# Optimization experiments

Measured on AMD Instinct MI355X. Metric: run time of the kernel, lower is better.

The kernel has to match this reference:

```python
import jax, jax.numpy as jnp
import numpy as np

GRID_SIZE = 5
SPLINE_ORDER = 3
COUPLING = 0.05
LN_EPS = 1e-5
BATCH = 1024
IN_DIM = 2048
HIDDEN = [4096, 4096, 2048]


def _knots():
    k = SPLINE_ORDER
    return np.concatenate([np.full(k, -1.0), np.linspace(-1.0, 1.0, GRID_SIZE + 1), np.full(k, 1.0)])


def bspline_basis(t):
    # Replicates the module's partial in-place Cox-de Boor recursion exactly:
    # after the loops, cols[0..4] are degree-3, col 5 degree-2, col 6 degree-1, col 7 degree-0.
    knots = _knots()
    k = SPLINE_ORDER
    n = len(knots) - k - 1  # 8
    cols = [jnp.where((t >= knots[i]) & (t < knots[i + 1]), 1.0, 0.0).astype(t.dtype)
            for i in range(min(n, len(knots) - 1))]
    for degree in range(1, min(k + 1, n)):
        for i in range(n - degree):
            denom1 = knots[i + degree] - knots[i]
            denom2 = knots[i + degree + 1] - knots[i + 1]
            term1 = ((t - knots[i]) / denom1) * cols[i] if denom1 > 1e-10 else 0.0
            term2 = (((knots[i + degree + 1] - t) / denom2) * cols[i + 1]
                     if (denom2 > 1e-10 and i + 1 < n) else 0.0)
            cols[i] = term1 + term2
    return jnp.stack(cols, axis=-1)  # [..., n]


def kan_activation(x, control_points, reg_weights):
    # x: [B, D]; control_points: [D, grid+order+1]; reg_weights: [D]
    t = jnp.tanh(x)
    basis = bspline_basis(t)  # [B, D, n]
    m = min(basis.shape[-1], control_points.shape[1])  # min(8, 9) = 8
    spline = jnp.einsum('bdn,dn->bd', basis[..., :m], control_points[:, :m])
    return jnp.clip(spline * reg_weights[None, :], -10.0, 10.0)


def _generators():
    sx = np.array([[0., 1.], [1., 0.]], np.float32)
    sy = np.array([[0., -1.], [1., 0.]], np.float32)
    sz = np.array([[1., 0.], [0., -1.]], np.float32)
    return np.stack([sx, sy, sz, np.eye(2, dtype=np.float32)])  # [4,2,2]

GENS = jnp.asarray(_generators())
GEN_DIAG = jnp.asarray(np.stack([np.diagonal(g) for g in _generators()]))  # [4,2]


def noncommutative_transform(x):
    # pairs of the flattened tensor, generator index cycles mod 4
    shape = x.shape
    flat = x.reshape(-1)
    P = flat.shape[0] // 2
    vec = flat[:2 * P].reshape(P, 2)
    ng = GENS.shape[0]
    if P % ng == 0:
        v = vec.reshape(P // ng, ng, 2)                      # [Q, 4, 2]
        gv = jnp.einsum('gij,qgj->qgi', GENS, v)
        vg = v * GEN_DIAG[None, :, :]
        comm = jnp.clip(gv - vg, -1.0, 1.0)
        out = (v + COUPLING * comm).reshape(-1)
    else:
        G = GENS[jnp.arange(P) % ng]
        gv = jnp.einsum('pij,pj->pi', G, vec)
        vg = vec * jnp.diagonal(G, axis1=-2, axis2=-1)
        comm = jnp.clip(gv - vg, -1.0, 1.0)
        out = (vec + COUPLING * comm).reshape(-1)
    if flat.shape[0] % 2 == 1:
        out = jnp.concatenate([out, flat[-1:]])
    return out.reshape(shape)


def setup_inputs() -> dict:
    key = jax.random.key(0)
    ks = jax.random.split(key, 16)
    inp = {'x': jax.random.normal(ks[0], (BATCH, IN_DIM), jnp.float32)}
    prev = IN_DIM
    ncp = GRID_SIZE + SPLINE_ORDER + 1  # 9
    for li, h in enumerate(HIDDEN, start=1):
        kw, kb, kc = jax.random.split(ks[li], 3)
        inp[f'W{li}'] = jax.random.normal(kw, (h, prev), jnp.float32) / np.sqrt(prev)
        inp[f'b{li}'] = jnp.zeros((h,), jnp.float32)
        inp[f'cp{li}'] = jax.random.normal(kc, (h, ncp), jnp.float32) * 0.1
        inp[f'rw{li}'] = jnp.full((h,), 0.5, jnp.float32)
        prev = h
    inp['W_out'] = jax.random.normal(ks[10], (IN_DIM, prev), jnp.float32) / np.sqrt(prev)
    inp['b_out'] = jnp.zeros((IN_DIM,), jnp.float32)
    return inp


def reference(x, W1, b1, cp1, rw1, W2, b2, cp2, rw2, W3, b3, cp3, rw3, W_out, b_out):
    # F.layer_norm over feature dim, no affine
    mu = jnp.mean(x, axis=-1, keepdims=True)
    var = jnp.var(x, axis=-1, keepdims=True)
    cur = (x - mu) / jnp.sqrt(var + LN_EPS)
    for W, b, cp, rw in ((W1, b1, cp1, rw1), (W2, b2, cp2, rw2), (W3, b3, cp3, rw3)):
        lin = cur @ W.T + b
        kan = kan_activation(lin, cp, rw)
        cur = noncommutative_transform(kan)  # dropout = identity in eval
    return cur @ W_out.T + b_out
```

## Files before the change

kernel.cpp:

```cpp
#include <hip/hip_runtime.h>

typedef __attribute__((ext_vector_type(8))) short bf16x8;
typedef __attribute__((ext_vector_type(4))) float f32x4;

__device__ __forceinline__ float b2f(unsigned short u) {
    union { unsigned int i; float f; } x; x.i = ((unsigned int)u) << 16; return x.f;
}
__device__ __forceinline__ unsigned short f2b(float f) {
    union { float f; unsigned int i; } x; x.f = f;
    unsigned int r = x.i + 0x7fffu + ((x.i >> 16) & 1u);
    return (unsigned short)(r >> 16);
}

__device__ __forceinline__ void gl16(unsigned short* l, const unsigned short* g) {
    __builtin_amdgcn_global_load_lds((__attribute__((address_space(1))) void*)g,
                                     (__attribute__((address_space(3))) void*)l, 16, 0, 0);
}

__device__ __forceinline__ float kan_spline(float t, const float* cpf, float rwf) {
    float c3 = (t >= -1.0f && t < -0.6f) ? 1.0f : 0.0f;
    float c4 = (t >= -0.6f && t < -0.2f) ? 1.0f : 0.0f;
    float c5 = (t >= -0.2f && t <  0.2f) ? 1.0f : 0.0f;
    float c6 = (t >=  0.2f && t <  0.6f) ? 1.0f : 0.0f;
    float c7 = (t >=  0.6f && t <  1.0f) ? 1.0f : 0.0f;
    float d2 = (-0.6f - t) * 2.5f * c3;
    float d3 = (t + 1.0f) * 2.5f * c3 + (-0.2f - t) * 2.5f * c4;
    float d4 = (t + 0.6f) * 2.5f * c4 + ( 0.2f - t) * 2.5f * c5;
    float d5 = (t + 0.2f) * 2.5f * c5 + ( 0.6f - t) * 2.5f * c6;
    float d6 = (t - 0.2f) * 2.5f * c6 + ( 1.0f - t) * 2.5f * c7;
    float e1 = (-0.6f - t) * 2.5f  * d2;
    float e2 = (t + 1.0f) * 2.5f  * d2 + (-0.2f - t) * 1.25f * d3;
    float e3 = (t + 1.0f) * 1.25f * d3 + ( 0.2f - t) * 1.25f * d4;
    float e4 = (t + 0.6f) * 1.25f * d4 + ( 0.6f - t) * 1.25f * d5;
    float e5 = (t + 0.2f) * 1.25f * d5 + ( 1.0f - t) * 1.25f * d6;
    const float r12 = 1.0f / 1.2f;
    float f0 = (-0.6f - t) * 2.5f  * e1;
    float f1 = (t + 1.0f) * 2.5f  * e1 + (-0.2f - t) * 1.25f * e2;
    float f2 = (t + 1.0f) * 1.25f * e2 + ( 0.2f - t) * r12   * e3;
    float f3 = (t + 1.0f) * r12   * e3 + ( 0.6f - t) * r12   * e4;
    float f4 = (t + 0.6f) * r12   * e4 + ( 1.0f - t) * r12   * e5;
    float sp = f0*cpf[0] + f1*cpf[1] + f2*cpf[2] + f3*cpf[3] + f4*cpf[4]
             + e5*cpf[5] + d6*cpf[6] + c7*cpf[7];
    float v = sp * rwf;
    return fminf(fmaxf(v, -10.0f), 10.0f);
}

__global__ void ln_stats_kernel(const float* __restrict__ x,
                                float* __restrict__ mu, float* __restrict__ rstd) {
    const int row = blockIdx.x;
    const float* p = x + (size_t)row * 2048 + threadIdx.x * 8;
    double s = 0.0, q = 0.0;
#pragma unroll
    for (int i = 0; i < 8; ++i) { float v = p[i]; s += v; q += (double)v * v; }
    for (int o = 32; o > 0; o >>= 1) { s += __shfl_down(s, o, 64); q += __shfl_down(q, o, 64); }
    __shared__ double shs[4], shq[4];
    const int lane = threadIdx.x & 63, w = threadIdx.x >> 6;
    if (lane == 0) { shs[w] = s; shq[w] = q; }
    __syncthreads();
    if (threadIdx.x == 0) {
        double S = shs[0] + shs[1] + shs[2] + shs[3];
        double Q = shq[0] + shq[1] + shq[2] + shq[3];
        double m = S / 2048.0;
        double var = Q / 2048.0 - m * m;
        mu[row] = (float)m;
        rstd[row] = (float)(1.0 / sqrt(var + 1e-5));
    }
}

__global__ void rowsum_kernel(const float* __restrict__ W,
                              float* __restrict__ S, int K) {
    const int lane = threadIdx.x & 63, w = threadIdx.x >> 6;
    const int row = blockIdx.x * 4 + w;
    const float* p = W + (size_t)row * K;
    double s = 0.0;
    for (int c = lane * 8; c < K; c += 512) {
#pragma unroll
        for (int i = 0; i < 8; ++i) s += p[c + i];
    }
    for (int o = 32; o > 0; o >>= 1) s += __shfl_down(s, o, 64);
    if (lane == 0) S[row] = (float)s;
}

__global__ void split2_kernel(const float* __restrict__ src,
                              unsigned short* __restrict__ dst, int C) {
    const int r = blockIdx.x;
    const int c = threadIdx.x * 8;
    const float* p = src + (size_t)r * C + c;
    float4 u0 = ((const float4*)p)[0];
    float4 u1 = ((const float4*)p)[1];
    float v[8] = {u0.x, u0.y, u0.z, u0.w, u1.x, u1.y, u1.z, u1.w};
    unsigned short hi[8], lo[8];
#pragma unroll
    for (int i = 0; i < 8; ++i) {
        hi[i] = f2b(v[i]);
        lo[i] = f2b(v[i] - b2f(hi[i]));
    }
    unsigned short* d = dst + (size_t)r * 2 * C + c;
    *(uint4*)d = *(const uint4*)hi;
    *(uint4*)(d + C) = *(const uint4*)lo;
}

__global__ void pre_all(const float* __restrict__ x, const float* __restrict__ W1,
                        float* __restrict__ mu, float* __restrict__ rstd,
                        float* __restrict__ S1,
                        unsigned short* __restrict__ Asplit,
                        unsigned short* __restrict__ W1b) {
    const int tid = threadIdx.x;
    const int lane = tid & 63, w = tid >> 6;
    const int c = tid * 8;
    __shared__ double shs[4], shq[4];
    if (blockIdx.x < 1024) {
        const int r = blockIdx.x;
        const float* p = x + (size_t)r * 2048 + c;
        float4 u0 = ((const float4*)p)[0];
        float4 u1 = ((const float4*)p)[1];
        float v[8] = {u0.x, u0.y, u0.z, u0.w, u1.x, u1.y, u1.z, u1.w};
        double s = 0.0, q = 0.0;
#pragma unroll
        for (int i = 0; i < 8; ++i) { s += v[i]; q += (double)v[i] * v[i]; }
        for (int o = 32; o > 0; o >>= 1) { s += __shfl_down(s, o, 64); q += __shfl_down(q, o, 64); }
        if (lane == 0) { shs[w] = s; shq[w] = q; }
        __syncthreads();
        if (tid == 0) {
            double S = shs[0] + shs[1] + shs[2] + shs[3];
            double Q = shq[0] + shq[1] + shq[2] + shq[3];
            double m = S / 2048.0;
            double var = Q / 2048.0 - m * m;
            mu[r] = (float)m;
            rstd[r] = (float)(1.0 / sqrt(var + 1e-5));
        }
        unsigned short hi[8], lo[8];
#pragma unroll
        for (int i = 0; i < 8; ++i) {
            hi[i] = f2b(v[i]);
            lo[i] = f2b(v[i] - b2f(hi[i]));
        }
        unsigned short* d = Asplit + (size_t)r * 4096 + c;
        *(uint4*)d = *(const uint4*)hi;
        *(uint4*)(d + 2048) = *(const uint4*)lo;
    } else {
        const int r = blockIdx.x - 1024;
        const float* p = W1 + (size_t)r * 2048 + c;
        float4 u0 = ((const float4*)p)[0];
        float4 u1 = ((const float4*)p)[1];
        float v[8] = {u0.x, u0.y, u0.z, u0.w, u1.x, u1.y, u1.z, u1.w};
        double s = 0.0;
#pragma unroll
        for (int i = 0; i < 8; ++i) s += v[i];
        for (int o = 32; o > 0; o >>= 1) s += __shfl_down(s, o, 64);
        if (lane == 0) shs[w] = s;
        __syncthreads();
        if (tid == 0) S1[r] = (float)(shs[0] + shs[1] + shs[2] + shs[3]);
        unsigned short hi[8], lo[8];
#pragma unroll
        for (int i = 0; i < 8; ++i) {
            hi[i] = f2b(v[i]);
            lo[i] = f2b(v[i] - b2f(hi[i]));
        }
        unsigned short* d = W1b + (size_t)r * 4096 + c;
        *(uint4*)d = *(const uint4*)hi;
        *(uint4*)(d + 2048) = *(const uint4*)lo;
    }
}

__global__ void cvt_kernel(const float* __restrict__ src,
                           unsigned short* __restrict__ dst) {
    const size_t i = ((size_t)blockIdx.x * 256 + threadIdx.x) * 8;
    float4 u0 = ((const float4*)(src + i))[0];
    float4 u1 = ((const float4*)(src + i))[1];
    float v[8] = {u0.x, u0.y, u0.z, u0.w, u1.x, u1.y, u1.z, u1.w};
    unsigned short t[8];
#pragma unroll
    for (int q = 0; q < 8; ++q) t[q] = f2b(v[q]);
    *(uint4*)(dst + i) = *(const uint4*)t;
}

__global__ void cvt2_kernel(const float* __restrict__ s1, unsigned short* __restrict__ d1,
                            int nb1, const float* __restrict__ s2,
                            unsigned short* __restrict__ d2) {
    const int b = blockIdx.x;
    const float* src = (b < nb1) ? s1 : s2;
    unsigned short* dst = (b < nb1) ? d1 : d2;
    const int bb = (b < nb1) ? b : b - nb1;
    const size_t i = ((size_t)bb * 256 + threadIdx.x) * 8;
    float4 u0 = ((const float4*)(src + i))[0];
    float4 u1 = ((const float4*)(src + i))[1];
    float v[8] = {u0.x, u0.y, u0.z, u0.w, u1.x, u1.y, u1.z, u1.w};
    unsigned short t[8];
#pragma unroll
    for (int q = 0; q < 8; ++q) t[q] = f2b(v[q]);
    *(uint4*)(dst + i) = *(const uint4*)t;
}

__global__ __launch_bounds__(512, 4)
void gemm_kan1(const unsigned short* __restrict__ Ab,
               const unsigned short* __restrict__ Bb,
               const float* __restrict__ bias, const float* __restrict__ cp,
               const float* __restrict__ rw, const float* __restrict__ mu,
               const float* __restrict__ rstd, const float* __restrict__ S1,
               unsigned short* __restrict__ outp,
               int Nld, int Klog, int lda, int ldb)
{
    constexpr int BM = 64, BN = 128;
    constexpr int ABASE = 0, BBASE = 4096;
    constexpr int BUF = 12288;
    __shared__ unsigned short lds[3 * BUF];

    const int tid  = threadIdx.x;
    const int lane = tid & 63;
    const int wid  = tid >> 6;

    const int gx = gridDim.x;
    int flat = blockIdx.y * gx + blockIdx.x;
    const int nwg = gx * gridDim.y;
    if ((nwg & 7) == 0) flat = (flat & 7) * (nwg >> 3) + (flat >> 3);
    const int bm = (flat % gx) * BM;
    const int bn = (flat / gx) * BN;

    const int wmo = (wid >> 2) * 32;
    const int wno = (wid & 3) * 32;
    const int fr = lane & 15;
    const int kq = lane >> 4;
    const int sxr = fr & 7;

    const int uA0 = tid;
    const int uB0 = tid, uB1 = tid + 512;
#define VLOG(u) ((((u) & 7)) ^ (((u) >> 3) & 7))
#define SRCC(u) (((VLOG(u) & 3) << 3) + ((VLOG(u) >> 2) * 2048))
    const size_t aoff0 = (size_t)(bm + (uA0 >> 3)) * lda + SRCC(uA0);
    const size_t boff0 = (size_t)(bn + (uB0 >> 3)) * ldb + SRCC(uB0);
    const size_t boff1 = (size_t)(bn + (uB1 >> 3)) * ldb + SRCC(uB1);
#undef SRCC
#undef VLOG

    f32x4 acc[2][2] = {};

#define STAGE(BSEL, K) do {                                           \
    unsigned short* l_ = &lds[(BSEL) * BUF];                          \
    gl16(l_ + ABASE + uA0 * 8, Ab + aoff0 + (K));                     \
    gl16(l_ + BBASE + uB0 * 8, Bb + boff0 + (K));                     \
    gl16(l_ + BBASE + uB1 * 8, Bb + boff1 + (K));                     \
} while (0)

    const int nt = Klog / 32;
    STAGE(0, 0);
    STAGE(1, 32);

    for (int t = 0; t < nt; ++t) {
        if (t + 1 < nt) asm volatile("s_waitcnt vmcnt(3)" ::: "memory");
        else            asm volatile("s_waitcnt vmcnt(0)" ::: "memory");
        __builtin_amdgcn_s_barrier();
        __builtin_amdgcn_sched_barrier(0);
        if (t + 2 < nt) STAGE((t + 2) % 3, (t + 2) * 32);
        const unsigned short* cl = &lds[(t % 3) * BUF];
        const int slH = ((kq ^ sxr)) << 3;
        const int slL = (((4 + kq) ^ sxr)) << 3;
        bf16x8 aH[2], aL[2], bH[2], bL[2];
#pragma unroll
        for (int i = 0; i < 2; ++i) {
            const int ro = ABASE + (wmo + i * 16 + fr) * 64;
            aH[i] = *(const bf16x8*)&cl[ro + slH];
            aL[i] = *(const bf16x8*)&cl[ro + slL];
        }
#pragma unroll
        for (int j = 0; j < 2; ++j) {
            const int ro = BBASE + (wno + j * 16 + fr) * 64;
            bH[j] = *(const bf16x8*)&cl[ro + slH];
            bL[j] = *(const bf16x8*)&cl[ro + slL];
        }
#pragma unroll
        for (int i = 0; i < 2; ++i)
#pragma unroll
            for (int j = 0; j < 2; ++j)
                acc[i][j] = __builtin_amdgcn_mfma_f32_16x16x32_bf16(aH[i], bH[j], acc[i][j], 0, 0, 0);
#pragma unroll
        for (int i = 0; i < 2; ++i)
#pragma unroll
            for (int j = 0; j < 2; ++j)
                acc[i][j] = __builtin_amdgcn_mfma_f32_16x16x32_bf16(aL[i], bH[j], acc[i][j], 0, 0, 0);
#pragma unroll
        for (int i = 0; i < 2; ++i)
#pragma unroll
            for (int j = 0; j < 2; ++j)
                acc[i][j] = __builtin_amdgcn_mfma_f32_16x16x32_bf16(aH[i], bL[j], acc[i][j], 0, 0, 0);
    }
#undef STAGE

    const int rowg = (lane >> 4) * 4;
#pragma unroll
    for (int j = 0; j < 2; ++j) {
        const int n = bn + wno + j * 16 + fr;
        const float bs = bias[n];
        float cpf[8];
#pragma unroll
        for (int q = 0; q < 8; ++q) cpf[q] = cp[(size_t)n * 9 + q];
        const float rwf = rw[n];
        const float s1 = S1[n];
        const int s = n & 7;
#pragma unroll
        for (int i = 0; i < 2; ++i) {
            const int m0 = bm + wmo + i * 16 + rowg;
#pragma unroll
            for (int r = 0; r < 4; ++r) {
                const int m = m0 + r;
                float v = acc[i][j][r];
                v = (v - mu[m] * s1) * rstd[m] + bs;
                v = kan_spline(tanhf(v), cpf, rwf);
                float p = __shfl_xor(v, 1, 64);
                p = fminf(fmaxf(p, -1.0f), 1.0f);
                if (s < 4) v += ((s == 2) ? -0.05f : 0.05f) * p;
                outp[(size_t)m * Nld + n] = f2b(v);
            }
        }
    }
}

template <int EPI>
__global__ __launch_bounds__(256, 2)
void gemm_kan2(const unsigned short* __restrict__ Ab,
               const unsigned short* __restrict__ Bb,
               const float* __restrict__ bias, const float* __restrict__ cp,
               const float* __restrict__ rw, const float* __restrict__ mu,
               const float* __restrict__ rstd, const float* __restrict__ S1,
               void* __restrict__ outp,
               int Nld, int n0, int Ktot, int lda, int ldb)
{
    constexpr int BM = 64, BN = 128, BK = 64;
    constexpr int ASZ = BM * BK;
    constexpr int BUF = ASZ + BN * BK;
    __shared__ unsigned short lds[3 * BUF];

    const int tid  = threadIdx.x;
    const int lane = tid & 63;
    const int wid  = tid >> 6;

    const int gx = gridDim.x;
    int flat = blockIdx.y * gx + blockIdx.x;
    const int nwg = gx * gridDim.y;
    if ((nwg & 7) == 0) flat = (flat & 7) * (nwg >> 3) + (flat >> 3);
    const int bm = (flat % gx) * BM;
    const int bn = (flat / gx) * BN;

    const int wmo = (wid >> 1) * 32;
    const int wno = (wid & 1) * 64;
    const int fr = lane & 15;
    const int kq = lane >> 4;
    const int sxr = fr & 7;

    const int uA0 = (wid << 7) + lane;
    const int uA1 = uA0 + 64;
    const int uB0 = (wid << 8) + lane;
    const int uB1 = uB0 + 64, uB2 = uB0 + 128, uB3 = uB0 + 192;
#define SRCOL(u) (((((u) & 7) ^ (((u) >> 3) & 7))) << 3)
    const size_t aoff0 = (size_t)(bm + (uA0 >> 3)) * lda + SRCOL(uA0);
    const size_t aoff1 = (size_t)(bm + (uA1 >> 3)) * lda + SRCOL(uA1);
    const size_t boff0 = (size_t)(bn + (uB0 >> 3)) * ldb + SRCOL(uB0);
    const size_t boff1 = (size_t)(bn + (uB1 >> 3)) * ldb + SRCOL(uB1);
    const size_t boff2 = (size_t)(bn + (uB2 >> 3)) * ldb + SRCOL(uB2);
    const size_t boff3 = (size_t)(bn + (uB3 >> 3)) * ldb + SRCOL(uB3);
#undef SRCOL

    f32x4 acc[2][4] = {};

#define STAGE(BSEL, AK, BKK) do {                                     \
    unsigned short* lA_ = &lds[(BSEL) * BUF];                         \
    unsigned short* lB_ = lA_ + ASZ;                                  \
    gl16(lA_ + uA0 * 8, Ab + aoff0 + (AK));                           \
    gl16(lA_ + uA1 * 8, Ab + aoff1 + (AK));                           \
    gl16(lB_ + uB0 * 8, Bb + boff0 + (BKK));                          \
    gl16(lB_ + uB1 * 8, Bb + boff1 + (BKK));                          \
    gl16(lB_ + uB2 * 8, Bb + boff2 + (BKK));                          \
    gl16(lB_ + uB3 * 8, Bb + boff3 + (BKK));                          \
} while (0)

    const int nt = Ktot / BK;
    STAGE(0, 0, 0);
    STAGE(1, BK, BK);

    for (int t = 0; t < nt; ++t) {
        if (t + 1 < nt) asm volatile("s_waitcnt vmcnt(6)" ::: "memory");
        else            asm volatile("s_waitcnt vmcnt(0)" ::: "memory");
        __builtin_amdgcn_s_barrier();
        __builtin_amdgcn_sched_barrier(0);
        if (t + 2 < nt) {
            const int kn = (t + 2) * BK;
            int ak = kn, bk = kn;
            if (EPI == 0) {
                ak = (kn < 4096) ? kn : kn - 4096;
                bk = (kn < 2048) ? kn : kn - 2048;
            }
            STAGE((t + 2) % 3, ak, bk);
        }
        const unsigned short* cl = &lds[(t % 3) * BUF];
#pragma unroll
        for (int s = 0; s < 2; ++s) {
            const int sl = ((((s << 2) + kq) ^ sxr)) << 3;
            bf16x8 aF[2], bF[4];
#pragma unroll
            for (int i = 0; i < 2; ++i)
                aF[i] = *(const bf16x8*)&cl[(wmo + i * 16 + fr) * BK + sl];
#pragma unroll
            for (int j = 0; j < 4; ++j)
                bF[j] = *(const bf16x8*)&cl[ASZ + (wno + j * 16 + fr) * BK + sl];
#pragma unroll
            for (int i = 0; i < 2; ++i)
#pragma unroll
                for (int j = 0; j < 4; ++j)
                    acc[i][j] = __builtin_amdgcn_mfma_f32_16x16x32_bf16(aF[i], bF[j], acc[i][j], 0, 0, 0);
        }
    }
#undef STAGE

    const int rowg = (lane >> 4) * 4;
#pragma unroll
    for (int j = 0; j < 4; ++j) {
        const int n = n0 + bn + wno + j * 16 + fr;
        const float bs = bias[n];
        float cpf[8], rwf = 0.0f, s1 = 0.0f;
        if (EPI < 2) {
#pragma unroll
            for (int q = 0; q < 8; ++q) cpf[q] = cp[(size_t)n * 9 + q];
            rwf = rw[n];
        }
        if (EPI == 0) s1 = S1[n];
        const int s = n & 7;
#pragma unroll
        for (int i = 0; i < 2; ++i) {
            const int m0 = bm + wmo + i * 16 + rowg;
#pragma unroll
            for (int r = 0; r < 4; ++r) {
                const int m = m0 + r;
                float v = acc[i][j][r];
                if (EPI == 0) v = (v - mu[m] * s1) * rstd[m] + bs;
                else          v += bs;
                if (EPI < 2) {
                    v = kan_spline(tanhf(v), cpf, rwf);
                    float p = __shfl_xor(v, 1, 64);
                    p = fminf(fmaxf(p, -1.0f), 1.0f);
                    if (s < 4) v += ((s == 2) ? -0.05f : 0.05f) * p;
                }
                if (EPI == 2) ((float*)outp)[(size_t)m * Nld + n] = v;
                else ((unsigned short*)outp)[(size_t)m * Nld + n] = f2b(v);
            }
        }
    }
}

template <int EPI, int BSRC>
__global__ __launch_bounds__(256, 2)
void gemm_kan(const void* __restrict__ Av, const void* __restrict__ Bv,
              const float* __restrict__ bias, const float* __restrict__ cp,
              const float* __restrict__ rw, const float* __restrict__ mu,
              const float* __restrict__ rstd, const float* __restrict__ S1,
              void* __restrict__ outp,
              int Nld, int n0, int Ktot, int lda, int ldb)
{
    constexpr int BM = 64, BN = 64, BK = 64, LDP = 72;
    constexpr bool SPL = (BSRC == 2);
    constexpr int OFF_B  = BM * LDP;
    constexpr int OFF_LO = (BM + BN) * LDP;
    __shared__ unsigned short lds[(SPL ? 2 : 1) * (BM + BN) * LDP];

    const int tid  = threadIdx.x;
    const int lane = tid & 63;
    const int wid  = tid >> 6;
    const int bm = blockIdx.x * BM;
    const int bn = blockIdx.y * BN;
    const int wmo = (wid >> 1) * 32;
    const int wno = (wid & 1) * 32;
    const int fr = lane & 15;
    const int kq = lane >> 4;
    const int sar = tid >> 3, sac = (tid & 7) << 3;
    const int sfr = tid >> 2, sfc = (tid & 3) << 4;

    f32x4 acc[2][2] = {};

    uint4 pA0 = {}, pA1 = {}, pB0 = {}, pB1 = {};
    const unsigned short* Ab = (const unsigned short*)Av;
    const unsigned short* Bb = (const unsigned short*)Bv;
    const size_t a0 = (size_t)(bm + sar) * lda + sac;
    const size_t a1 = (size_t)(bm + 32 + sar) * lda + sac;
    const size_t b0 = (size_t)(bn + sar) * ldb + sac;
    const size_t b1 = (size_t)(bn + 32 + sar) * ldb + sac;
    if constexpr (BSRC == 0) {
        pA0 = *(const uint4*)(Ab + a0);
        pA1 = *(const uint4*)(Ab + a1);
        pB0 = *(const uint4*)(Bb + b0);
        pB1 = *(const uint4*)(Bb + b1);
    }

    for (int k0 = 0; k0 < Ktot; k0 += BK) {
        if constexpr (BSRC == 0) {
            *(uint4*)&lds[sar * LDP + sac] = pA0;
            *(uint4*)&lds[(32 + sar) * LDP + sac] = pA1;
            *(uint4*)&lds[OFF_B + sar * LDP + sac] = pB0;
            *(uint4*)&lds[OFF_B + (32 + sar) * LDP + sac] = pB1;
        } else {
            {
                const float* g = (const float*)Bv + (size_t)(bn + sfr) * ldb + k0 + sfc;
                float4 u0 = ((const float4*)g)[0];
                float4 u1 = ((const float4*)g)[1];
                float4 u2 = ((const float4*)g)[2];
                float4 u3 = ((const float4*)g)[3];
                float v[16] = {u0.x,u0.y,u0.z,u0.w, u1.x,u1.y,u1.z,u1.w,
                               u2.x,u2.y,u2.z,u2.w, u3.x,u3.y,u3.z,u3.w};
                unsigned short hi[16], lo[16];
#pragma unroll
                for (int i = 0; i < 16; ++i) {
                    hi[i] = f2b(v[i]);
                    if (SPL) lo[i] = f2b(v[i] - b2f(hi[i]));
                }
                unsigned short* d = &lds[OFF_B + sfr * LDP + sfc];
                ((uint4*)d)[0] = *(const uint4*)&hi[0];
                ((uint4*)d)[1] = *(const uint4*)&hi[8];
                if constexpr (SPL) {
                    unsigned short* dl = d + OFF_LO;
                    ((uint4*)dl)[0] = *(const uint4*)&lo[0];
                    ((uint4*)dl)[1] = *(const uint4*)&lo[8];
                }
            }
            if constexpr (SPL) {
                const float* g = (const float*)Av + (size_t)(bm + sfr) * lda + k0 + sfc;
                float4 u0 = ((const float4*)g)[0];
                float4 u1 = ((const float4*)g)[1];
                float4 u2 = ((const float4*)g)[2];
                float4 u3 = ((const float4*)g)[3];
                float v[16] = {u0.x,u0.y,u0.z,u0.w, u1.x,u1.y,u1.z,u1.w,
                               u2.x,u2.y,u2.z,u2.w, u3.x,u3.y,u3.z,u3.w};
                unsigned short hi[16], lo[16];
#pragma unroll
                for (int i = 0; i < 16; ++i) {
                    hi[i] = f2b(v[i]);
                    lo[i] = f2b(v[i] - b2f(hi[i]));
                }
                unsigned short* d = &lds[sfr * LDP + sfc];
                ((uint4*)d)[0] = *(const uint4*)&hi[0];
                ((uint4*)d)[1] = *(const uint4*)&hi[8];
                unsigned short* dl = d + OFF_LO;
                ((uint4*)dl)[0] = *(const uint4*)&lo[0];
                ((uint4*)dl)[1] = *(const uint4*)&lo[8];
            } else {
                *(uint4*)&lds[sar * LDP + sac] = *(const uint4*)(Ab + a0 + k0);
                *(uint4*)&lds[(32 + sar) * LDP + sac] = *(const uint4*)(Ab + a1 + k0);
            }
        }
        __syncthreads();
        if constexpr (BSRC == 0) {
            if (k0 + BK < Ktot) {
                const int kn = k0 + BK;
                const int ak = (EPI == 0) ? (kn < 4096 ? kn : kn - 4096) : kn;
                const int bk = (EPI == 0) ? (kn < 2048 ? kn : kn - 2048) : kn;
                pA0 = *(const uint4*)(Ab + a0 + ak);
                pA1 = *(const uint4*)(Ab + a1 + ak);
                pB0 = *(const uint4*)(Bb + b0 + bk);
                pB1 = *(const uint4*)(Bb + b1 + bk);
            }
        }
#pragma unroll
        for (int s = 0; s < 2; ++s) {
            const int cc = (s * 4 + kq) << 3;
            bf16x8 aF[2], bF[2];
#pragma unroll
            for (int i = 0; i < 2; ++i)
                aF[i] = *(const bf16x8*)&lds[(wmo + i * 16 + fr) * LDP + cc];
#pragma unroll
            for (int j = 0; j < 2; ++j)
                bF[j] = *(const bf16x8*)&lds[OFF_B + (wno + j * 16 + fr) * LDP + cc];
#pragma unroll
            for (int i = 0; i < 2; ++i)
#pragma unroll
                for (int j = 0; j < 2; ++j)
                    acc[i][j] = __builtin_amdgcn_mfma_f32_16x16x32_bf16(aF[i], bF[j], acc[i][j], 0, 0, 0);
            if constexpr (SPL) {
                bf16x8 aL[2], bL[2];
#pragma unroll
                for (int i = 0; i < 2; ++i)
                    aL[i] = *(const bf16x8*)&lds[OFF_LO + (wmo + i * 16 + fr) * LDP + cc];
#pragma unroll
                for (int i = 0; i < 2; ++i)
#pragma unroll
                    for (int j = 0; j < 2; ++j)
                        acc[i][j] = __builtin_amdgcn_mfma_f32_16x16x32_bf16(aL[i], bF[j], acc[i][j], 0, 0, 0);
#pragma unroll
                for (int j = 0; j < 2; ++j)
                    bL[j] = *(const bf16x8*)&lds[OFF_LO + OFF_B + (wno + j * 16 + fr) * LDP + cc];
#pragma unroll
                for (int i = 0; i < 2; ++i)
#pragma unroll
                    for (int j = 0; j < 2; ++j)
                        acc[i][j] = __builtin_amdgcn_mfma_f32_16x16x32_bf16(aF[i], bL[j], acc[i][j], 0, 0, 0);
            }
        }
        __syncthreads();
    }

    const int rowg = (lane >> 4) * 4;
#pragma unroll
    for (int j = 0; j < 2; ++j) {
        const int n = n0 + bn + wno + j * 16 + fr;
        const float bs = bias[n];
        float cpf[8], rwf = 0.0f, s1 = 0.0f;
        if (EPI < 2) {
#pragma unroll
            for (int q = 0; q < 8; ++q) cpf[q] = cp[(size_t)n * 9 + q];
            rwf = rw[n];
        }
        if (EPI == 0) s1 = S1[n];
        const int s = n & 7;
#pragma unroll
        for (int i = 0; i < 2; ++i) {
            const int m0 = bm + wmo + i * 16 + rowg;
#pragma unroll
            for (int r = 0; r < 4; ++r) {
                const int m = m0 + r;
                float v = acc[i][j][r];
                if (EPI == 0) v = (v - mu[m] * s1) * rstd[m] + bs;
                else          v += bs;
                if (EPI < 2) {
                    v = kan_spline(tanhf(v), cpf, rwf);
                    float p = __shfl_xor(v, 1, 64);
                    p = fminf(fmaxf(p, -1.0f), 1.0f);
                    if (s < 4) v += ((s == 2) ? -0.05f : 0.05f) * p;
                }
                if (EPI == 2) ((float*)outp)[(size_t)m * Nld + n] = v;
                else ((unsigned short*)outp)[(size_t)m * Nld + n] = f2b(v);
            }
        }
    }
}

extern "C" void kernel_launch(void* const* d_in, const int* in_sizes, int n_in,
                              void* d_out, int out_size, void* d_ws, size_t ws_size,
                              hipStream_t stream) {
    const float* x    = (const float*)d_in[0];
    const float* W1   = (const float*)d_in[1];
    const float* b1   = (const float*)d_in[2];
    const float* cp1  = (const float*)d_in[3];
    const float* rw1  = (const float*)d_in[4];
    const float* W2   = (const float*)d_in[5];
    const float* b2   = (const float*)d_in[6];
    const float* cp2  = (const float*)d_in[7];
    const float* rw2  = (const float*)d_in[8];
    const float* W3   = (const float*)d_in[9];
    const float* b3   = (const float*)d_in[10];
    const float* cp3  = (const float*)d_in[11];
    const float* rw3  = (const float*)d_in[12];
    const float* Wout = (const float*)d_in[13];
    const float* bout = (const float*)d_in[14];

    char* ws = (char*)d_ws;
    float* mu   = (float*)(ws);
    float* rstd = (float*)(ws + 4096);
    float* S1   = (float*)(ws + 8192);
    unsigned short* A2 = (unsigned short*)(ws + 32768);
    unsigned short* A3 = (unsigned short*)(ws + 32768 + 8388608);
    unsigned short* A4 = A2;
    unsigned short* Asplit = A3;
    unsigned short* Wb = (unsigned short*)(ws + 32768 + 2 * 8388608);
    const size_t NEED_FULL = 32768 + 2 * 8388608 + 33554432;
    const size_t NEED_HALF = 32768 + 2 * 8388608 + 16777216;

    if (ws_size >= NEED_FULL) {
        pre_all<<<5120, 256, 0, stream>>>(x, W1, mu, rstd, S1, Asplit, Wb);
        gemm_kan1<<<dim3(16, 32), 512, 0, stream>>>(
            Asplit, Wb, b1, cp1, rw1, mu, rstd, S1, A2, 4096, 2048, 4096, 4096);
        cvt_kernel<<<8192, 256, 0, stream>>>(W2, Wb);
        gemm_kan2<1><<<dim3(16, 32), 256, 0, stream>>>(
            A2, Wb, b2, cp2, rw2, nullptr, nullptr, nullptr, A3, 4096, 0, 4096, 4096, 4096);
        cvt2_kernel<<<6144, 256, 0, stream>>>(W3, Wb, 4096, Wout, Wb + 8388608);
        gemm_kan2<1><<<dim3(16, 16), 256, 0, stream>>>(
            A3, Wb, b3, cp3, rw3, nullptr, nullptr, nullptr, A4, 2048, 0, 4096, 4096, 4096);
        gemm_kan2<2><<<dim3(16, 16), 256, 0, stream>>>(
            A4, Wb + 8388608, bout, nullptr, nullptr, nullptr, nullptr, nullptr, d_out, 2048, 0, 2048, 2048, 2048);
    } else if (ws_size >= NEED_HALF) {
        ln_stats_kernel<<<1024, 256, 0, stream>>>(x, mu, rstd);
        rowsum_kernel<<<1024, 256, 0, stream>>>(W1, S1, 2048);
        split2_kernel<<<1024, 256, 0, stream>>>(x, Asplit, 2048);
        for (int h = 0; h < 2; ++h) {
            split2_kernel<<<2048, 256, 0, stream>>>(W1 + (size_t)h * 2048 * 2048, Wb, 2048);
            gemm_kan2<0><<<dim3(16, 16), 256, 0, stream>>>(
                Asplit, Wb, b1, cp1, rw1, mu, rstd, S1, A2, 4096, h * 2048, 6144, 4096, 4096);
        }
        for (int h = 0; h < 2; ++h) {
            cvt_kernel<<<4096, 256, 0, stream>>>(W2 + (size_t)h * 2048 * 4096, Wb);
            gemm_kan2<1><<<dim3(16, 16), 256, 0, stream>>>(
                A2, Wb, b2, cp2, rw2, nullptr, nullptr, nullptr, A3, 4096, h * 2048, 4096, 4096, 4096);
        }
        cvt_kernel<<<4096, 256, 0, stream>>>(W3, Wb);
        gemm_kan2<1><<<dim3(16, 16), 256, 0, stream>>>(
            A3, Wb, b3, cp3, rw3, nullptr, nullptr, nullptr, A4, 2048, 0, 4096, 4096, 4096);
        cvt_kernel<<<2048, 256, 0, stream>>>(Wout, Wb);
        gemm_kan2<2><<<dim3(16, 16), 256, 0, stream>>>(
            A4, Wb, bout, nullptr, nullptr, nullptr, nullptr, nullptr, d_out, 2048, 0, 2048, 2048, 2048);
    } else {
        ln_stats_kernel<<<1024, 256, 0, stream>>>(x, mu, rstd);
        rowsum_kernel<<<1024, 256, 0, stream>>>(W1, S1, 2048);
        gemm_kan<0, 2><<<dim3(16, 64), 256, 0, stream>>>(
            x, W1, b1, cp1, rw1, mu, rstd, S1, A2, 4096, 0, 2048, 2048, 2048);
        gemm_kan<1, 1><<<dim3(16, 64), 256, 0, stream>>>(
            A2, W2, b2, cp2, rw2, nullptr, nullptr, nullptr, A3, 4096, 0, 4096, 4096, 4096);
        gemm_kan<1, 1><<<dim3(16, 32), 256, 0, stream>>>(
            A3, W3, b3, cp3, rw3, nullptr, nullptr, nullptr, A4, 2048, 0, 4096, 4096, 4096);
        gemm_kan<2, 1><<<dim3(16, 32), 256, 0, stream>>>(
            A4, Wout, bout, nullptr, nullptr, nullptr, nullptr, nullptr, d_out, 2048, 0, 2048, 2048, 2048);
    }
}
```

Baseline: 377.5 us.

## Add 512-thread 8-wave GEMM kernel for layer-2 KAN GEMM

Adds gemm_kan3, a 512-thread variant of the 64x128x64 tiled bf16 MFMA GEMM. Each of its 8 waves computes a 32x32 sub-tile, giving a 2x2 MFMA accumulator per wave. It also adds an XCD-aware block remapping of the flattened block index, and it drops the layernorm-correction epilogue terms that layer 2 does not need. Layer 2 switches to the new kernel to raise wave-level parallelism and latency hiding. The cost is less MFMA work per wave between barriers, relative to the LDS traffic each wave issues.

```diff
diff --git a/kernel.cpp b/kernel.cpp
--- a/kernel.cpp
+++ b/kernel.cpp
@@ -316,6 +316,117 @@
 }
 
 template <int EPI>
+__global__ __launch_bounds__(512, 4)
+void gemm_kan3(const unsigned short* __restrict__ Ab,
+               const unsigned short* __restrict__ Bb,
+               const float* __restrict__ bias, const float* __restrict__ cp,
+               const float* __restrict__ rw,
+               void* __restrict__ outp,
+               int Nld, int Ktot, int lda, int ldb)
+{
+    constexpr int BM = 64, BN = 128, BK = 64;
+    constexpr int ASZ = BM * BK;
+    constexpr int BUF = ASZ + BN * BK;
+    __shared__ unsigned short lds[3 * BUF];
+
+    const int tid  = threadIdx.x;
+    const int lane = tid & 63;
+    const int wid  = tid >> 6;
+
+    const int gx = gridDim.x;
+    int flat = blockIdx.y * gx + blockIdx.x;
+    const int nwg = gx * gridDim.y;
+    if ((nwg & 7) == 0) flat = (flat & 7) * (nwg >> 3) + (flat >> 3);
+    const int bm = (flat % gx) * BM;
+    const int bn = (flat / gx) * BN;
+
+    const int wmo = (wid >> 2) * 32;
+    const int wno = (wid & 3) * 32;
+    const int fr = lane & 15;
+    const int kq = lane >> 4;
+    const int sxr = fr & 7;
+
+    const int uA0 = tid;
+    const int uB0 = tid, uB1 = tid + 512;
+#define SRCOL(u) (((((u) & 7) ^ (((u) >> 3) & 7))) << 3)
+    const size_t aoff0 = (size_t)(bm + (uA0 >> 3)) * lda + SRCOL(uA0);
+    const size_t boff0 = (size_t)(bn + (uB0 >> 3)) * ldb + SRCOL(uB0);
+    const size_t boff1 = (size_t)(bn + (uB1 >> 3)) * ldb + SRCOL(uB1);
+#undef SRCOL
+
+    f32x4 acc[2][2] = {};
+
+#define STAGE(BSEL, K) do {                                           \
+    unsigned short* lA_ = &lds[(BSEL) * BUF];                         \
+    unsigned short* lB_ = lA_ + ASZ;                                  \
+    gl16(lA_ + uA0 * 8, Ab + aoff0 + (K));                            \
+    gl16(lB_ + uB0 * 8, Bb + boff0 + (K));                            \
+    gl16(lB_ + uB1 * 8, Bb + boff1 + (K));                            \
+} while (0)
+
+    const int nt = Ktot / BK;
+    STAGE(0, 0);
+    STAGE(1, BK);
+
+    for (int t = 0; t < nt; ++t) {
+        if (t + 1 < nt) asm volatile("s_waitcnt vmcnt(3)" ::: "memory");
+        else            asm volatile("s_waitcnt vmcnt(0)" ::: "memory");
+        __builtin_amdgcn_s_barrier();
+        __builtin_amdgcn_sched_barrier(0);
+        if (t + 2 < nt) STAGE((t + 2) % 3, (t + 2) * BK);
+        const unsigned short* cl = &lds[(t % 3) * BUF];
+#pragma unroll
+        for (int s = 0; s < 2; ++s) {
+            const int sl = ((((s << 2) + kq) ^ sxr)) << 3;
+            bf16x8 aF[2], bF[2];
+#pragma unroll
+            for (int i = 0; i < 2; ++i)
+                aF[i] = *(const bf16x8*)&cl[(wmo + i * 16 + fr) * BK + sl];
+#pragma unroll
+            for (int j = 0; j < 2; ++j)
+                bF[j] = *(const bf16x8*)&cl[ASZ + (wno + j * 16 + fr) * BK + sl];
+#pragma unroll
+            for (int i = 0; i < 2; ++i)
+#pragma unroll
+                for (int j = 0; j < 2; ++j)
+                    acc[i][j] = __builtin_amdgcn_mfma_f32_16x16x32_bf16(aF[i], bF[j], acc[i][j], 0, 0, 0);
+        }
+    }
+#undef STAGE
+
+    const int rowg = (lane >> 4) * 4;
+#pragma unroll
+    for (int j = 0; j < 2; ++j) {
+        const int n = bn + wno + j * 16 + fr;
+        const float bs = bias[n];
+        float cpf[8], rwf = 0.0f;
+        if (EPI < 2) {
+#pragma unroll
+            for (int q = 0; q < 8; ++q) cpf[q] = cp[(size_t)n * 9 + q];
+            rwf = rw[n];
+        }
+        const int s = n & 7;
+#pragma unroll
+        for (int i = 0; i < 2; ++i) {
+            const int m0 = bm + wmo + i * 16 + rowg;
+#pragma unroll
+            for (int r = 0; r < 4; ++r) {
+                const int m = m0 + r;
+                float v = acc[i][j][r] + bs;
+                if (EPI < 2) {
+                    v = kan_spline(tanhf(v), cpf, rwf);
+                    float p = __shfl_xor(v, 1, 64);
+                    p = fminf(fmaxf(p, -1.0f), 1.0f);
+                    if (s < 4) v += ((s == 2) ? -0.05f : 0.05f) * p;
+                }
+                if (EPI == 2) ((float*)outp)[(size_t)m * Nld + n] = v;
+                else ((unsigned short*)outp)[(size_t)m * Nld + n] = f2b(v);
+            }
+        }
+    }
+}
+
+template <int EPI>
 __global__ __launch_bounds__(256, 2)
 void gemm_kan2(const unsigned short* __restrict__ Ab,
                const unsigned short* __restrict__ Bb,
@@ -665,8 +776,8 @@
         gemm_kan1<<<dim3(16, 32), 512, 0, stream>>>(
             Asplit, Wb, b1, cp1, rw1, mu, rstd, S1, A2, 4096, 2048, 4096, 4096);
         cvt_kernel<<<8192, 256, 0, stream>>>(W2, Wb);
-        gemm_kan2<1><<<dim3(16, 32), 256, 0, stream>>>(
-            A2, Wb, b2, cp2, rw2, nullptr, nullptr, nullptr, A3, 4096, 0, 4096, 4096, 4096);
+        gemm_kan3<1><<<dim3(16, 32), 512, 0, stream>>>(
+            A2, Wb, b2, cp2, rw2, A3, 4096, 4096, 4096, 4096);
         cvt2_kernel<<<6144, 256, 0, stream>>>(W3, Wb, 4096, Wout, Wb + 8388608);
         gemm_kan2<1><<<dim3(16, 16), 256, 0, stream>>>(
             A3, Wb, b3, cp3, rw3, nullptr, nullptr, nullptr, A4, 2048, 0, 4096, 4096, 4096);
```

After: 378.5 us. No clear change (+0.3%).
